# Optimization experiments

Hardware: AMD Instinct MI355X
Metric: run time of the kernel (lower is better)

## Reference

```python
import jax, jax.numpy as jnp
import numpy as np
from jax import lax

GROUPS = 4
DILATIONS = (1, 6, 12, 18)
PADDINGS = (1, 6, 12, 18)


def setup_inputs() -> dict:
    key = jax.random.key(0)
    k1, k2, k3 = jax.random.split(key, 3)
    x = jax.random.normal(k1, (8, 64, 320, 320), dtype=jnp.float32)
    weight = jax.random.normal(k2, (64, 16, 3, 3), dtype=jnp.float32) * 0.05
    bias = jax.random.normal(k3, (64,), dtype=jnp.float32) * 0.05
    return {"x": x, "weight": weight, "bias": bias}


def reference(x, weight, bias):
    # x: [b, c, h, w]; channels split into GROUPS groups of c/GROUPS each.
    # Group g is convolved (3x3, stride 1) with dilation DILATIONS[g] and
    # zero-padding PADDINGS[g] (= 'same'), using weight group g of shape
    # [out_ch/GROUPS, c/GROUPS, 3, 3]. Outputs concatenated along channels.
    b, c, h, w = x.shape
    out_ch = weight.shape[0]
    xg = x.reshape(b, GROUPS, c // GROUPS, h, w)
    wg = weight.reshape(GROUPS, out_ch // GROUPS, weight.shape[1], 3, 3)
    dn = lax.conv_dimension_numbers(xg[:, 0].shape, wg[0].shape, ("NCHW", "OIHW", "NCHW"))
    outs = []
    for g in range(GROUPS):
        p, d = PADDINGS[g], DILATIONS[g]
        outs.append(
            lax.conv_general_dilated(
                xg[:, g], wg[g],
                window_strides=(1, 1),
                padding=[(p, p), (p, p)],
                rhs_dilation=(d, d),
                dimension_numbers=dn,
            )
        )
    out = jnp.concatenate(outs, axis=1)  # [b, out_ch, h, w]
    return out + bias[None, :, None, None]
```

## Files before the change

kernel.cpp:

```cpp
#include <hip/hip_runtime.h>
#include <hip/hip_bf16.h>

typedef short short8 __attribute__((ext_vector_type(8)));
typedef short short4_t __attribute__((ext_vector_type(4)));
typedef float floatx4 __attribute__((ext_vector_type(4)));
typedef unsigned short ushort_t;
typedef unsigned int uint32;

#define H 320
#define W 320
#define CG 16
#define NCH 64
#define HW (H * W)
#define CGP 20
#define HALFW 160

__device__ __forceinline__ ushort_t f2bf(float f) {
  unsigned u = __float_as_uint(f);
  return (ushort_t)((u + 0x7FFFu + ((u >> 16) & 1u)) >> 16);
}

__device__ __forceinline__ void barrier_lgkm() {
  asm volatile("s_waitcnt lgkmcnt(0)" ::: "memory");
  __builtin_amdgcn_s_barrier();
}

template<int G>
__device__ __forceinline__ void conv_group(
    const float* __restrict__ x, const float* __restrict__ wgt,
    const float* __restrict__ bias, float* __restrict__ out,
    ushort_t* lds, int bx) {
  constexpr int DIL   = (G == 0) ? 1 : (G == 1) ? 6 : (G == 2) ? 12 : 18;
  constexpr int KOFF  = DIL & 1;
  constexpr int SHIFT = DIL + KOFF;
  constexpr int WH    = (HALFW + 2 * DIL + KOFF + 1) & ~1;
  constexpr int NP    = (WH + 63) / 64;
  constexpr int WKS   = 16 * DIL;
  constexpr int RPW   = (H + DIL - 1) / DIL;
  constexpr int Q     = (RPW + 3) / 4;
  constexpr int CPW   = (G == 0) ? 12 : (G == 1) ? 2 : 1;
  constexpr int L     = (Q + CPW - 1) / CPW;

  const int tid = threadIdx.x;
  ushort_t* tile = lds;
  ushort_t* swt  = lds + 6 * WH * CGP;
  uint32* swt32  = (uint32*)swt;

#pragma unroll
  for (int k = 0; k < 5; ++k) {
    const int s = tid + k * 256;
    const int jp = s & 3, oc = (s >> 2) & 15, zz = (s >> 6) & 3, t = s >> 8;
    const int tp = 2 * t + (zz >> 1);
    uint32 pk = 0;
    if (tp < 9) {
      const float* wp = wgt + ((size_t)(G * CG + oc) * CG + (zz & 1) * 8 + 2 * jp) * 9 + tp;
      pk = (uint32)f2bf(wp[0]) | ((uint32)f2bf(wp[9]) << 16);
    }
    swt32[s] = pk;
  }
  __syncthreads();

  const int lane = tid & 63;
  const int wv   = tid >> 6;
  const int z = lane >> 4, icq = z & 1, pxl = lane & 15;
  short8 aw[5];
#pragma unroll
  for (int t = 0; t < 5; ++t) aw[t] = *(const short8*)&swt[((t * 4 + z) * 16 + pxl) * 8];
  const float bb = bias[G * CG + pxl];

  const int walk  = bx % WKS;
  const int chunk = bx / WKS;
  const int r  = walk % DIL;
  const int wb = ((walk / DIL) & 1) * HALFW;
  const int b  = walk / (2 * DIL);
  const int q0 = chunk * L;
  const int qend = (q0 + L < Q) ? q0 + L : Q;

  bool zm[NP]; bool inb[NP]; int gofs[NP];
#pragma unroll
  for (int p = 0; p < NP; ++p) {
    const int c = 64 * p + lane;
    inb[p] = (c < WH);
    const int gc = wb + c - SHIFT;
    zm[p] = inb[p] & (gc >= 0) & (gc < W);
    gofs[p] = gc < 0 ? 0 : (gc >= W ? W - 1 : gc);
  }
  const float* chb = x + (size_t)(b * NCH + G * CG + 4 * wv) * HW;

  auto LOADR = [&](int rho, float (&rg)[NP][4]) {
    const int yy = rho * DIL + r;
    const int yyc = yy < 0 ? 0 : (yy >= H ? H - 1 : yy);
    const float* rp = chb + (size_t)yyc * W;
#pragma unroll
    for (int p = 0; p < NP; ++p)
#pragma unroll
      for (int k = 0; k < 4; ++k)
        rg[p][k] = rp[(size_t)k * HW + gofs[p]];
  };

  auto CVTR = [&](int rho, int slot, float (&rg)[NP][4]) {
    const int yy = rho * DIL + r;
    const bool rv = (yy >= 0) & (yy < H);
#pragma unroll
    for (int p = 0; p < NP; ++p) {
      const bool m = rv & zm[p];
      const __hip_bfloat162 h01 = __float22bfloat162_rn(make_float2(rg[p][0], rg[p][1]));
      const __hip_bfloat162 h23 = __float22bfloat162_rn(make_float2(rg[p][2], rg[p][3]));
      uint2 pk;
      pk.x = m ? *(const uint32*)&h01 : 0u;
      pk.y = m ? *(const uint32*)&h23 : 0u;
      if (inb[p]) {
        const int c = 64 * p + lane;
        *(uint2*)&tile[(size_t)(slot * WH + c) * CGP + wv * 4] = pk;
      }
    }
  };

  auto COMPUTE = [&](int q, int m6) {
    const int y = (4 * q + wv) * DIL + r;
    if (y >= H) return;
    const int zh = z >> 1;
    float* outb = out + (size_t)(b * NCH + G * CG + pxl) * HW + (size_t)y * W + wb + 4 * z;
    const ushort_t* rowp[5];
#pragma unroll
    for (int t = 0; t < 5; ++t) {
      const int tp = 2 * t + zh;
      const int ky = tp < 9 ? tp / 3 : 0;
      const int kx = tp < 9 ? tp - ky * 3 : 0;
      int s = m6 + wv + ky; s -= (s >= 6) ? 6 : 0;
      rowp[t] = tile + (size_t)s * (WH * CGP) + (size_t)(pxl + kx * DIL + KOFF) * CGP + icq * 8;
    }
#pragma unroll 2
    for (int ti = 0; ti < HALFW / 16; ++ti) {
      floatx4 acc = {0.f, 0.f, 0.f, 0.f};
#pragma unroll
      for (int t = 0; t < 5; ++t) {
        const ushort_t* pf = rowp[t] + ti * 16 * CGP;
        const short4_t lo = *(const short4_t*)pf;
        const short4_t hi = *(const short4_t*)(pf + 4);
        const short8 bf = {lo[0], lo[1], lo[2], lo[3], hi[0], hi[1], hi[2], hi[3]};
        acc = __builtin_amdgcn_mfma_f32_16x16x32_bf16(bf, aw[t], acc, 0, 0, 0);
      }
      floatx4 st = {acc[0] + bb, acc[1] + bb, acc[2] + bb, acc[3] + bb};
      __builtin_nontemporal_store(st, (floatx4*)(outb + ti * 16));
    }
  };

  auto wrap6 = [](int v) { return v >= 6 ? v - 6 : v; };
  int m6 = (4 * q0 + 5) % 6;

  {
    float ra[NP][4], rb[NP][4];
    LOADR(4 * q0 - 1, ra); LOADR(4 * q0 + 0, rb);
    CVTR(4 * q0 - 1, wrap6(m6 + 0), ra); CVTR(4 * q0 + 0, wrap6(m6 + 1), rb);
    LOADR(4 * q0 + 1, ra); LOADR(4 * q0 + 2, rb);
    CVTR(4 * q0 + 1, wrap6(m6 + 2), ra); CVTR(4 * q0 + 2, wrap6(m6 + 3), rb);
    LOADR(4 * q0 + 3, ra); LOADR(4 * q0 + 4, rb);
    CVTR(4 * q0 + 3, wrap6(m6 + 4), ra); CVTR(4 * q0 + 4, wrap6(m6 + 5), rb);
  }
  barrier_lgkm();

#pragma unroll 1
  for (int q = q0; q < qend - 1; ++q) {
    float ra[NP][4], rb[NP][4], rc[NP][4], rd[NP][4];
    LOADR(4 * q + 5, ra); LOADR(4 * q + 6, rb);
    LOADR(4 * q + 7, rc); LOADR(4 * q + 8, rd);
    COMPUTE(q, m6);
    barrier_lgkm();
    CVTR(4 * q + 5, m6,            ra);
    CVTR(4 * q + 6, wrap6(m6 + 1), rb);
    CVTR(4 * q + 7, wrap6(m6 + 2), rc);
    CVTR(4 * q + 8, wrap6(m6 + 3), rd);
    barrier_lgkm();
    m6 = wrap6(m6 + 4);
  }
  COMPUTE(qend - 1, m6);
}

extern "C" __global__ void __launch_bounds__(256, 3) conv_all(
    const float* __restrict__ x, const float* __restrict__ wgt,
    const float* __restrict__ bias, float* __restrict__ out) {
  extern __shared__ ushort_t lds[];
  const int bid = blockIdx.x;
  if (bid < 288)      conv_group<3>(x, wgt, bias, out, lds, bid);
  else if (bid < 480) conv_group<2>(x, wgt, bias, out, lds, bid - 288);
  else if (bid < 672) conv_group<1>(x, wgt, bias, out, lds, bid - 480);
  else                conv_group<0>(x, wgt, bias, out, lds, bid - 672);
}

extern "C" void kernel_launch(void* const* d_in, const int* in_sizes, int n_in,
                              void* d_out, int out_size, void* d_ws, size_t ws_size,
                              hipStream_t stream) {
  const float* x    = (const float*)d_in[0];
  const float* wgt  = (const float*)d_in[1];
  const float* bias = (const float*)d_in[2];
  float* out        = (float*)d_out;

  const size_t lds_bytes = (size_t)(6 * 196 * CGP + 5 * 4 * 16 * 8) * 2;
  conv_all<<<dim3(864), dim3(256), lds_bytes, stream>>>(x, wgt, bias, out);
}
```

Before: 102.8 us.

## Vectorize row staging with mod-4 column layout, load weights directly, split work finer

Row staging now has each lane read a float4 per channel and scatter the four columns into a mod-4 interleaved LDS layout. This replaces the earlier scalar per-column loads held in registers across compute, so loads are no longer overlapped with MFMA. Weights are read straight from global memory into registers rather than staged through LDS, which removes a barrier and some LDS space. The grid grows from 864 to 2064 blocks with smaller row chunks per block, improving load balance and occupancy at the cost of more halo rows per block. Output stores become regular stores instead of nontemporal.

Measured after the change: 125.3 us. +21.9%, slower.

```diff
diff --git a/kernel.cpp b/kernel.cpp
--- a/kernel.cpp
+++ b/kernel.cpp
@@ -29,43 +29,34 @@
 __device__ __forceinline__ void conv_group(
     const float* __restrict__ x, const float* __restrict__ wgt,
     const float* __restrict__ bias, float* __restrict__ out,
-    ushort_t* lds, int bx) {
+    ushort_t* tile, int bx) {
   constexpr int DIL   = (G == 0) ? 1 : (G == 1) ? 6 : (G == 2) ? 12 : 18;
-  constexpr int KOFF  = DIL & 1;
-  constexpr int SHIFT = DIL + KOFF;
-  constexpr int WH    = (HALFW + 2 * DIL + KOFF + 1) & ~1;
-  constexpr int NP    = (WH + 63) / 64;
+  constexpr int S4    = (G == 0) ? 4 : (G == 1) ? 8 : (G == 2) ? 12 : 20;
+  constexpr int QW    = (G == 0) ? 43 : (G == 1) ? 45 : (G == 2) ? 47 : 51;
+  constexpr int WH4   = 4 * QW;
+  constexpr int KOFF4 = S4 - DIL;
   constexpr int WKS   = 16 * DIL;
   constexpr int RPW   = (H + DIL - 1) / DIL;
-  constexpr int Q     = (RPW + 3) / 4;
-  constexpr int CPW   = (G == 0) ? 12 : (G == 1) ? 2 : 1;
-  constexpr int L     = (Q + CPW - 1) / CPW;
+  constexpr int QT    = (RPW + 3) / 4;
+  constexpr int CPW   = (G == 0) ? 27 : (G == 1) ? 5 : (G == 2) ? 3 : 2;
+  constexpr int L     = (QT + CPW - 1) / CPW;
 
-  const int tid = threadIdx.x;
-  ushort_t* tile = lds;
-  ushort_t* swt  = lds + 6 * WH * CGP;
-  uint32* swt32  = (uint32*)swt;
-
-#pragma unroll
-  for (int k = 0; k < 5; ++k) {
-    const int s = tid + k * 256;
-    const int jp = s & 3, oc = (s >> 2) & 15, zz = (s >> 6) & 3, t = s >> 8;
-    const int tp = 2 * t + (zz >> 1);
-    uint32 pk = 0;
-    if (tp < 9) {
-      const float* wp = wgt + ((size_t)(G * CG + oc) * CG + (zz & 1) * 8 + 2 * jp) * 9 + tp;
-      pk = (uint32)f2bf(wp[0]) | ((uint32)f2bf(wp[9]) << 16);
-    }
-    swt32[s] = pk;
-  }
-  __syncthreads();
-
+  const int tid  = threadIdx.x;
   const int lane = tid & 63;
   const int wv   = tid >> 6;
-  const int z = lane >> 4, icq = z & 1, pxl = lane & 15;
+  const int pxl = lane & 15, z = lane >> 4, icq = z & 1, zh = z >> 1;
+
   short8 aw[5];
 #pragma unroll
-  for (int t = 0; t < 5; ++t) aw[t] = *(const short8*)&swt[((t * 4 + z) * 16 + pxl) * 8];
+  for (int t = 0; t < 5; ++t) {
+    const int tp = 2 * t + zh;
+#pragma unroll
+    for (int jj = 0; jj < 8; ++jj) {
+      float v = 0.f;
+      if (tp < 9) v = wgt[((size_t)(G * CG + pxl) * CG + icq * 8 + jj) * 9 + tp];
+      aw[t][jj] = (short)f2bf(v);
+    }
+  }
   const float bb = bias[G * CG + pxl];
 
   const int walk  = bx % WKS;
@@ -74,44 +65,35 @@
   const int wb = ((walk / DIL) & 1) * HALFW;
   const int b  = walk / (2 * DIL);
   const int q0 = chunk * L;
-  const int qend = (q0 + L < Q) ? q0 + L : Q;
+  const int qend = (q0 + L < QT) ? q0 + L : QT;
+  if (q0 >= qend) return;
 
-  bool zm[NP]; bool inb[NP]; int gofs[NP];
-#pragma unroll
-  for (int p = 0; p < NP; ++p) {
-    const int c = 64 * p + lane;
-    inb[p] = (c < WH);
-    const int gc = wb + c - SHIFT;
-    zm[p] = inb[p] & (gc >= 0) & (gc < W);
-    gofs[p] = gc < 0 ? 0 : (gc >= W ? W - 1 : gc);
-  }
+  const bool act   = lane < QW;
+  const int  gq    = wb - S4 + 4 * lane;
+  const bool cvld  = (gq >= 0) & (gq < W);
+  const int  gcl   = gq < 0 ? 0 : (gq > W - 4 ? W - 4 : gq);
   const float* chb = x + (size_t)(b * NCH + G * CG + 4 * wv) * HW;
 
-  auto LOADR = [&](int rho, float (&rg)[NP][4]) {
-    const int yy = rho * DIL + r;
-    const int yyc = yy < 0 ? 0 : (yy >= H ? H - 1 : yy);
-    const float* rp = chb + (size_t)yyc * W;
-#pragma unroll
-    for (int p = 0; p < NP; ++p)
-#pragma unroll
-      for (int k = 0; k < 4; ++k)
-        rg[p][k] = rp[(size_t)k * HW + gofs[p]];
-  };
-
-  auto CVTR = [&](int rho, int slot, float (&rg)[NP][4]) {
+  auto STAGER = [&](int rho, int slot) {
     const int yy = rho * DIL + r;
     const bool rv = (yy >= 0) & (yy < H);
+    const int yyc = yy < 0 ? 0 : (yy >= H ? H - 1 : yy);
+    const float* rowb = chb + (size_t)yyc * W + gcl;
+    if (act) {
+      const floatx4 p0 = *(const floatx4*)(rowb);
+      const floatx4 p1 = *(const floatx4*)(rowb + HW);
+      const floatx4 p2 = *(const floatx4*)(rowb + 2 * HW);
+      const floatx4 p3 = *(const floatx4*)(rowb + 3 * HW);
+      const bool m = rv & cvld;
+      ushort_t* colp = tile + ((size_t)slot * WH4 + lane) * CGP + 4 * wv;
 #pragma unroll
-    for (int p = 0; p < NP; ++p) {
-      const bool m = rv & zm[p];
-      const __hip_bfloat162 h01 = __float22bfloat162_rn(make_float2(rg[p][0], rg[p][1]));
-      const __hip_bfloat162 h23 = __float22bfloat162_rn(make_float2(rg[p][2], rg[p][3]));
-      uint2 pk;
-      pk.x = m ? *(const uint32*)&h01 : 0u;
-      pk.y = m ? *(const uint32*)&h23 : 0u;
-      if (inb[p]) {
-        const int c = 64 * p + lane;
-        *(uint2*)&tile[(size_t)(slot * WH + c) * CGP + wv * 4] = pk;
+      for (int cc = 0; cc < 4; ++cc) {
+        const __hip_bfloat162 h01 = __float22bfloat162_rn(make_float2(p0[cc], p1[cc]));
+        const __hip_bfloat162 h23 = __float22bfloat162_rn(make_float2(p2[cc], p3[cc]));
+        uint2 pk;
+        pk.x = m ? *(const uint32*)&h01 : 0u;
+        pk.y = m ? *(const uint32*)&h23 : 0u;
+        *(uint2*)(colp + (size_t)cc * QW * CGP) = pk;
       }
     }
   };
@@ -119,7 +101,6 @@
   auto COMPUTE = [&](int q, int m6) {
     const int y = (4 * q + wv) * DIL + r;
     if (y >= H) return;
-    const int zh = z >> 1;
     float* outb = out + (size_t)(b * NCH + G * CG + pxl) * HW + (size_t)y * W + wb + 4 * z;
     const ushort_t* rowp[5];
 #pragma unroll
@@ -128,53 +109,44 @@
       const int ky = tp < 9 ? tp / 3 : 0;
       const int kx = tp < 9 ? tp - ky * 3 : 0;
       int s = m6 + wv + ky; s -= (s >= 6) ? 6 : 0;
-      rowp[t] = tile + (size_t)s * (WH * CGP) + (size_t)(pxl + kx * DIL + KOFF) * CGP + icq * 8;
+      const int ct = pxl + kx * DIL + KOFF4;
+      const int idx0 = (ct & 3) * QW + (ct >> 2);
+      rowp[t] = tile + ((size_t)s * WH4 + idx0) * CGP + icq * 8;
     }
 #pragma unroll 2
     for (int ti = 0; ti < HALFW / 16; ++ti) {
       floatx4 acc = {0.f, 0.f, 0.f, 0.f};
 #pragma unroll
       for (int t = 0; t < 5; ++t) {
-        const ushort_t* pf = rowp[t] + ti * 16 * CGP;
+        const ushort_t* pf = rowp[t] + ti * 4 * CGP;
         const short4_t lo = *(const short4_t*)pf;
         const short4_t hi = *(const short4_t*)(pf + 4);
         const short8 bf = {lo[0], lo[1], lo[2], lo[3], hi[0], hi[1], hi[2], hi[3]};
         acc = __builtin_amdgcn_mfma_f32_16x16x32_bf16(bf, aw[t], acc, 0, 0, 0);
       }
-      floatx4 st = {acc[0] + bb, acc[1] + bb, acc[2] + bb, acc[3] + bb};
-      __builtin_nontemporal_store(st, (floatx4*)(outb + ti * 16));
+      const floatx4 st = {acc[0] + bb, acc[1] + bb, acc[2] + bb, acc[3] + bb};
+      *(floatx4*)(outb + ti * 16) = st;
     }
   };
 
   auto wrap6 = [](int v) { return v >= 6 ? v - 6 : v; };
   int m6 = (4 * q0 + 5) % 6;
 
-  {
-    float ra[NP][4], rb[NP][4];
-    LOADR(4 * q0 - 1, ra); LOADR(4 * q0 + 0, rb);
-    CVTR(4 * q0 - 1, wrap6(m6 + 0), ra); CVTR(4 * q0 + 0, wrap6(m6 + 1), rb);
-    LOADR(4 * q0 + 1, ra); LOADR(4 * q0 + 2, rb);
-    CVTR(4 * q0 + 1, wrap6(m6 + 2), ra); CVTR(4 * q0 + 2, wrap6(m6 + 3), rb);
-    LOADR(4 * q0 + 3, ra); LOADR(4 * q0 + 4, rb);
-    CVTR(4 * q0 + 3, wrap6(m6 + 4), ra); CVTR(4 * q0 + 4, wrap6(m6 + 5), rb);
-  }
+#pragma unroll
+  for (int j = 0; j < 6; ++j) STAGER(4 * q0 - 1 + j, wrap6(m6 + j));
   barrier_lgkm();
 
 #pragma unroll 1
-  for (int q = q0; q < qend - 1; ++q) {
-    float ra[NP][4], rb[NP][4], rc[NP][4], rd[NP][4];
-    LOADR(4 * q + 5, ra); LOADR(4 * q + 6, rb);
-    LOADR(4 * q + 7, rc); LOADR(4 * q + 8, rd);
+  for (int q = q0; q < qend; ++q) {
     COMPUTE(q, m6);
-    barrier_lgkm();
-    CVTR(4 * q + 5, m6,            ra);
-    CVTR(4 * q + 6, wrap6(m6 + 1), rb);
-    CVTR(4 * q + 7, wrap6(m6 + 2), rc);
-    CVTR(4 * q + 8, wrap6(m6 + 3), rd);
-    barrier_lgkm();
-    m6 = wrap6(m6 + 4);
+    if (q + 1 < qend) {
+      barrier_lgkm();
+#pragma unroll
+      for (int j = 0; j < 4; ++j) STAGER(4 * q + 5 + j, wrap6(m6 + j));
+      barrier_lgkm();
+      m6 = wrap6(m6 + 4);
+    }
   }
-  COMPUTE(qend - 1, m6);
 }
 
 extern "C" __global__ void __launch_bounds__(256, 3) conv_all(
@@ -182,10 +154,10 @@
     const float* __restrict__ bias, float* __restrict__ out) {
   extern __shared__ ushort_t lds[];
   const int bid = blockIdx.x;
-  if (bid < 288)      conv_group<3>(x, wgt, bias, out, lds, bid);
-  else if (bid < 480) conv_group<2>(x, wgt, bias, out, lds, bid - 288);
-  else if (bid < 672) conv_group<1>(x, wgt, bias, out, lds, bid - 480);
-  else                conv_group<0>(x, wgt, bias, out, lds, bid - 672);
+  if (bid < 576)       conv_group<3>(x, wgt, bias, out, lds, bid);
+  else if (bid < 1152) conv_group<2>(x, wgt, bias, out, lds, bid - 576);
+  else if (bid < 1632) conv_group<1>(x, wgt, bias, out, lds, bid - 1152);
+  else                 conv_group<0>(x, wgt, bias, out, lds, bid - 1632);
 }
 
 extern "C" void kernel_launch(void* const* d_in, const int* in_sizes, int n_in,
@@ -196,6 +168,6 @@
   const float* bias = (const float*)d_in[2];
   float* out        = (float*)d_out;
 
-  const size_t lds_bytes = (size_t)(6 * 196 * CGP + 5 * 4 * 16 * 8) * 2;
-  conv_all<<<dim3(864), dim3(256), lds_bytes, stream>>>(x, wgt, bias, out);
+  const size_t lds_bytes = (size_t)6 * 204 * CGP * 2;
+  conv_all<<<dim3(2064), dim3(256), lds_bytes, stream>>>(x, wgt, bias, out);
 }
```
